# Performance work log

Hardware: AMD Instinct MI355X
Metric: run time of the kernel (lower is better)

The kernel has to match this reference:

```python
import jax, jax.numpy as jnp
import numpy as np

N = 100000      # num nodes
E = 1600000     # num edges (no self-loops; forward appends N self-loops)
DIN = 256       # in_channels
H = 1           # heads
C = 64          # out_channels per head
NEG = 0.2       # leaky_relu negative slope
NID = N // 10   # number of ID nodes


def setup_inputs() -> dict:
    key = jax.random.key(0)
    ks = jax.random.split(key, 7)
    x = jax.random.normal(ks[0], (N, DIN), jnp.float32)
    src = jax.random.randint(ks[1], (E,), 0, N, dtype=jnp.int32)
    off = jax.random.randint(ks[2], (E,), 1, N, dtype=jnp.int32)
    dst = ((src.astype(jnp.int64) + off.astype(jnp.int64)) % N).astype(jnp.int32)  # guarantees no self-loops
    edge_index = jnp.stack([src, dst])  # [2, E], row0 = source j, row1 = target i
    node_id = jax.random.randint(ks[3], (NID,), 0, N, dtype=jnp.int32)
    g = float(1.0 / np.sqrt(DIN))  # glorot-ish scale
    W = jax.random.uniform(ks[4], (DIN, H * C), jnp.float32, -g, g)
    W_id = jax.random.uniform(ks[5], (DIN, H * C), jnp.float32, -g, g)
    att = jax.random.uniform(ks[6], (1, H, 2 * C), jnp.float32, -g, g)
    return dict(x=x, edge_index=edge_index, node_id=node_id, W=W, W_id=W_id, att=att)


def _gat_id_forward(x, W, W_id, att, edge_index, node_id):
    # ID-aware transform: x @ W, plus extra W_id contribution added at id nodes
    x_id = x[node_id] @ W_id                      # [NID, H*C]
    h = x @ W                                     # [N, H*C]
    h = h.at[node_id].add(x_id)
    # add self-loops (inputs contain none)
    loops = jnp.arange(N, dtype=edge_index.dtype)
    src = jnp.concatenate([edge_index[0], loops])  # source j
    dst = jnp.concatenate([edge_index[1], loops])  # target i
    hr = h.reshape(N, H, C)
    xi = hr[dst]                                   # [Et, H, C]
    xj = hr[src]                                   # [Et, H, C]
    # alpha = (cat(x_i, x_j) * att).sum(-1)
    alpha = (xi * att[:, :, :C]).sum(-1) + (xj * att[:, :, C:]).sum(-1)  # [Et, H]
    alpha = jax.nn.leaky_relu(alpha, NEG)
    # segment softmax over target node (every node has a self-loop -> no empty segments)
    m = jax.ops.segment_max(alpha, dst, num_segments=N)
    alpha = jnp.exp(alpha - m[dst])
    s = jax.ops.segment_sum(alpha, dst, num_segments=N)
    alpha = alpha / (s[dst] + 1e-16)
    # dropout p=0 / eval mode -> no-op
    out = jax.ops.segment_sum(xj * alpha[:, :, None], dst, num_segments=N)  # [N, H, C]
    return out.reshape(N, H * C)  # concat=True, bias=False


def reference(x, edge_index, node_id, W, W_id, att):
    return _gat_id_forward(x, W, W_id, att, edge_index, node_id)
```

## Files before the change

kernel.cpp:

```cpp
#include <hip/hip_runtime.h>
#include <hip/hip_bf16.h>

#define N_NODES 100000
#define E_EDGES 1600000
#define DIN 256
#define C_OUT 64
#define NID_CNT 10000
#define NEG 0.2f
#define NBUCK 391
#define CAP 4608
#define GEMM_BLOCKS 391
#define BIN_BLOCKS 121
#define BIN_EPB 13224
#define BIN_ITERS 26

typedef short bf16x8 __attribute__((ext_vector_type(8)));
typedef float f32x4  __attribute__((ext_vector_type(4)));

__device__ __forceinline__ float lrelu(float x) { return x > 0.f ? x : NEG * x; }
__device__ __forceinline__ unsigned short f2bs(float f) {
    __hip_bfloat16 b = __float2bfloat16(f);
    return *reinterpret_cast<unsigned short*>(&b);
}
__device__ __forceinline__ bf16x8 pack8(float4 a, float4 b) {
    bf16x8 r;
    r[0] = (short)f2bs(a.x); r[1] = (short)f2bs(a.y);
    r[2] = (short)f2bs(a.z); r[3] = (short)f2bs(a.w);
    r[4] = (short)f2bs(b.x); r[5] = (short)f2bs(b.y);
    r[6] = (short)f2bs(b.z); r[7] = (short)f2bs(b.w);
    return r;
}
__device__ __forceinline__ float2 unpk2(unsigned u) {
    return make_float2(__uint_as_float(u << 16), __uint_as_float(u & 0xffff0000u));
}

__global__ __launch_bounds__(256) void k_zero(float* __restrict__ cnt,
                                              int* __restrict__ bkcur) {
    const int t = blockIdx.x * 256 + threadIdx.x;
    if (t < N_NODES) cnt[t] = 0.f;
    if (t < NBUCK) bkcur[t] = t * CAP;
}

__global__ __launch_bounds__(256) void k_prep(const float* __restrict__ W,
                                              const float* __restrict__ Wid,
                                              unsigned short* __restrict__ WtG,
                                              unsigned short* __restrict__ WidtG,
                                              const int* __restrict__ nid,
                                              float* __restrict__ cnt) {
    const int b = blockIdx.x;
    const int tid = threadIdx.x;
    if (b < 128) {
        const int t = b * 256 + tid;
        const int mat = t >> 14;
        const int r = t & 16383;
        const int k = r >> 6, c = r & 63;
        if (mat == 0) WtG[c * DIN + k] = f2bs(W[(long)k * C_OUT + c]);
        else          WidtG[c * DIN + k] = f2bs(Wid[(long)k * C_OUT + c]);
    } else {
        const int t = (b - 128) * 256 + tid;
        if (t < NID_CNT) atomicAdd(&cnt[nid[t]], 1.0f);
    }
}

__global__ __launch_bounds__(512, 4) void k_mega(const float* __restrict__ x,
                                                 const unsigned short* __restrict__ WtG,
                                                 const unsigned short* __restrict__ WidtG,
                                                 const float* __restrict__ cnt,
                                                 const float* __restrict__ att,
                                                 __hip_bfloat16* __restrict__ hb,
                                                 float* __restrict__ ad,
                                                 float* __restrict__ as,
                                                 const int* __restrict__ ei,
                                                 int* __restrict__ bkcur,
                                                 int2* __restrict__ binned) {
    __shared__ __align__(16) char smem[66560];
    const int blk = blockIdx.x;
    const int tid = threadIdx.x;

    if (blk < GEMM_BLOCKS) {
        char* wlds = smem;
        float* cnt_lds = (float*)(smem + 65536);
        const int w = tid >> 6, l = tid & 63;
        const int g = l >> 4, cl = l & 15;
        const int r0 = blk * 256;

        #pragma unroll
        for (int i = 0; i < 4; ++i) {
            int f = tid + i * 512;
            int c = f >> 5, s = f & 31;
            int byte = c * 512 + ((s ^ (c & 7)) << 4);
            *(bf16x8*)(wlds + byte)         = *(const bf16x8*)(WtG + (long)c * DIN + s * 8);
            *(bf16x8*)(wlds + 32768 + byte) = *(const bf16x8*)(WidtG + (long)c * DIN + s * 8);
        }
        if (tid < 256) cnt_lds[tid] = (r0 + tid < N_NODES) ? cnt[r0 + tid] : 0.f;
        __syncthreads();

        f32x4 acc1[2][4] = {};
        f32x4 acc2[2][4] = {};

        const int row0 = r0 + w * 32 + cl;
        const float* xp0 = x + (long)min(row0, N_NODES - 1) * DIN + g * 8;
        const float* xp1 = x + (long)min(row0 + 16, N_NODES - 1) * DIN + g * 8;

        float4 xb[2][4];
        xb[0][0] = *(const float4*)(xp0);
        xb[0][1] = *(const float4*)(xp0 + 4);
        xb[0][2] = *(const float4*)(xp1);
        xb[0][3] = *(const float4*)(xp1 + 4);
        #pragma unroll
        for (int kt = 0; kt < 8; ++kt) {
            if (kt < 7) {
                const int nb = (kt + 1) & 1;
                xb[nb][0] = *(const float4*)(xp0 + (kt + 1) * 32);
                xb[nb][1] = *(const float4*)(xp0 + (kt + 1) * 32 + 4);
                xb[nb][2] = *(const float4*)(xp1 + (kt + 1) * 32);
                xb[nb][3] = *(const float4*)(xp1 + (kt + 1) * 32 + 4);
            }
            const int cb = kt & 1;
            bf16x8 a0 = pack8(xb[cb][0], xb[cb][1]);
            bf16x8 a1 = pack8(xb[cb][2], xb[cb][3]);
            #pragma unroll
            for (int ct = 0; ct < 4; ++ct) {
                int c = ct * 16 + cl;
                int byte = c * 512 + (((kt * 4 + g) ^ (c & 7)) << 4);
                bf16x8 bw = *(const bf16x8*)(wlds + byte);
                bf16x8 bi = *(const bf16x8*)(wlds + 32768 + byte);
                acc1[0][ct] = __builtin_amdgcn_mfma_f32_16x16x32_bf16(a0, bw, acc1[0][ct], 0, 0, 0);
                acc1[1][ct] = __builtin_amdgcn_mfma_f32_16x16x32_bf16(a1, bw, acc1[1][ct], 0, 0, 0);
                acc2[0][ct] = __builtin_amdgcn_mfma_f32_16x16x32_bf16(a0, bi, acc2[0][ct], 0, 0, 0);
                acc2[1][ct] = __builtin_amdgcn_mfma_f32_16x16x32_bf16(a1, bi, acc2[1][ct], 0, 0, 0);
            }
        }
        __syncthreads();

        float attv1[4], attv2[4];
        #pragma unroll
        for (int ct = 0; ct < 4; ++ct) {
            attv1[ct] = att[ct * 16 + cl];
            attv2[ct] = att[C_OUT + ct * 16 + cl];
        }
        unsigned short* hbt = (unsigned short*)wlds;
        #pragma unroll
        for (int rt = 0; rt < 2; ++rt) {
            #pragma unroll
            for (int reg = 0; reg < 4; ++reg) {
                const int rbl = w * 32 + rt * 16 + g * 4 + reg;
                const float cv = cnt_lds[rbl];
                float pd = 0.f, ps = 0.f;
                #pragma unroll
                for (int ct = 0; ct < 4; ++ct) {
                    float hv = acc1[rt][ct][reg] + cv * acc2[rt][ct][reg];
                    pd += hv * attv1[ct];
                    ps += hv * attv2[ct];
                    hbt[rbl * 72 + ct * 16 + cl] = f2bs(hv);
                }
                #pragma unroll
                for (int o = 1; o < 16; o <<= 1) {
                    pd += __shfl_xor(pd, o, 64);
                    ps += __shfl_xor(ps, o, 64);
                }
                if (cl == 0) {
                    int grow = r0 + rbl;
                    if (grow < N_NODES) { ad[grow] = pd; as[grow] = ps; }
                }
            }
        }
        __syncthreads();
        #pragma unroll
        for (int i = 0; i < 4; ++i) {
            int f = tid + i * 512;
            int row = f >> 3, s = f & 7;
            int grow = r0 + row;
            if (grow < N_NODES) {
                bf16x8 v = *(const bf16x8*)(wlds + row * 144 + s * 16);
                *(bf16x8*)((unsigned short*)hb + (long)grow * C_OUT + s * 8) = v;
            }
        }
    } else {
        int* cnt_s = (int*)smem;
        int* base  = cnt_s + NBUCK;
        int* lcur  = base + NBUCK;
        const int b2 = blk - GEMM_BLOCKS;
        const int e0 = b2 * BIN_EPB;
        const int e1 = min(e0 + BIN_EPB, E_EDGES);
        for (int i = tid; i < NBUCK; i += 512) cnt_s[i] = 0;
        __syncthreads();
        int se[BIN_ITERS], de[BIN_ITERS];
        #pragma unroll
        for (int j = 0; j < BIN_ITERS; ++j) {
            int e = e0 + j * 512 + tid;
            if (e < e1) {
                se[j] = ei[e];
                de[j] = ei[E_EDGES + e];
                atomicAdd(&cnt_s[de[j] >> 8], 1);
            } else de[j] = -1;
        }
        __syncthreads();
        for (int i = tid; i < NBUCK; i += 512) {
            base[i] = cnt_s[i] ? atomicAdd(&bkcur[i], cnt_s[i]) : 0;
            lcur[i] = 0;
        }
        __syncthreads();
        #pragma unroll
        for (int j = 0; j < BIN_ITERS; ++j) {
            if (de[j] >= 0) {
                int bb = de[j] >> 8;
                int r = atomicAdd(&lcur[bb], 1);
                binned[base[bb] + r] = make_int2(se[j], de[j]);
            }
        }
    }
}

__global__ __launch_bounds__(256) void k_place(const int2* __restrict__ binned,
                                               const int* __restrict__ bkcur,
                                               int* __restrict__ csr,
                                               int* __restrict__ cur) {
    __shared__ int ncnt[256];
    __shared__ int tmp[256];
    __shared__ int ncur[256];
    const int tid = threadIdx.x;
    const int b = blockIdx.x;
    const int lo = b * CAP;
    const int n = bkcur[b] - lo;
    const int node0 = b << 8;
    ncnt[tid] = 0;
    __syncthreads();
    for (int e = tid; e < n; e += 256)
        atomicAdd(&ncnt[binned[lo + e].y - node0], 1);
    __syncthreads();
    const int v = ncnt[tid];
    tmp[tid] = v;
    __syncthreads();
    for (int o = 1; o < 256; o <<= 1) {
        int t = (tid >= o) ? tmp[tid - o] : 0;
        __syncthreads();
        tmp[tid] += t;
        __syncthreads();
    }
    const int incl = tmp[tid];
    if (node0 + tid < N_NODES) cur[node0 + tid] = lo + incl;
    ncur[tid] = incl - v;
    __syncthreads();
    for (int e = tid; e < n; e += 256) {
        int2 p = binned[lo + e];
        int r = atomicAdd(&ncur[p.y - node0], 1);
        csr[lo + r] = p.x;
    }
}

__global__ __launch_bounds__(256) void k_gather(const int* __restrict__ cur,
                                                const int* __restrict__ csr,
                                                const unsigned* __restrict__ hb2,
                                                const float* __restrict__ ad,
                                                const float* __restrict__ as,
                                                float* __restrict__ out) {
    const int lane = threadIdx.x & 63;
    const int lg = lane & 31;
    const int gb = lane & 32;
    const int i = blockIdx.x * 8 + ((threadIdx.x >> 6) << 1) + (lane >> 5);
    if (i >= N_NODES) return;
    const int end   = cur[i];
    const int start = (i & 255) ? cur[i - 1] : (i >> 8) * CAP;
    const int deg   = end - start;
    const float adi = ad[i];
    const float asi = as[i];
    float2 acc;
    float den;
    if (deg <= 32) {
        int s = 0; float a = -1e30f;
        if (lg < deg) { s = csr[start + lg]; a = as[s]; }
        float mx = fmaxf(a, asi);
        #pragma unroll
        for (int o = 16; o > 0; o >>= 1) mx = fmaxf(mx, __shfl_xor(mx, o, 64));
        const float m = lrelu(adi + mx);
        float w = (lg < deg) ? __expf(lrelu(adi + a) - m) : 0.f;
        const float wself = __expf(lrelu(adi + asi) - m);
        float wsum = w;
        #pragma unroll
        for (int o = 16; o > 0; o >>= 1) wsum += __shfl_xor(wsum, o, 64);
        den = wself + wsum;
        float2 hv = unpk2(hb2[(long)i * 32 + lg]);
        acc = make_float2(wself * hv.x, wself * hv.y);
        int j = 0;
        for (; j + 4 <= deg; j += 4) {
            int   s0 = __shfl(s, gb + j, 64),     s1 = __shfl(s, gb + j + 1, 64),
                  s2 = __shfl(s, gb + j + 2, 64), s3 = __shfl(s, gb + j + 3, 64);
            float w0 = __shfl(w, gb + j, 64),     w1 = __shfl(w, gb + j + 1, 64),
                  w2 = __shfl(w, gb + j + 2, 64), w3 = __shfl(w, gb + j + 3, 64);
            float2 h0 = unpk2(hb2[(long)s0 * 32 + lg]);
            float2 h1 = unpk2(hb2[(long)s1 * 32 + lg]);
            float2 h2 = unpk2(hb2[(long)s2 * 32 + lg]);
            float2 h3 = unpk2(hb2[(long)s3 * 32 + lg]);
            acc.x += w0 * h0.x; acc.y += w0 * h0.y;
            acc.x += w1 * h1.x; acc.y += w1 * h1.y;
            acc.x += w2 * h2.x; acc.y += w2 * h2.y;
            acc.x += w3 * h3.x; acc.y += w3 * h3.y;
        }
        for (; j < deg; ++j) {
            int   sj = __shfl(s, gb + j, 64);
            float wj = __shfl(w, gb + j, 64);
            float2 hj = unpk2(hb2[(long)sj * 32 + lg]);
            acc.x += wj * hj.x; acc.y += wj * hj.y;
        }
    } else {
        float mx = asi;
        for (int b = 0; b < deg; b += 32) {
            int idx = b + lg;
            if (idx < deg) mx = fmaxf(mx, as[csr[start + idx]]);
        }
        #pragma unroll
        for (int o = 16; o > 0; o >>= 1) mx = fmaxf(mx, __shfl_xor(mx, o, 64));
        const float m = lrelu(adi + mx);
        const float wself = __expf(lrelu(adi + asi) - m);
        float2 hv = unpk2(hb2[(long)i * 32 + lg]);
        acc = make_float2(wself * hv.x, wself * hv.y);
        den = wself;
        for (int b = 0; b < deg; b += 32) {
            int idx = b + lg;
            int s = 0; float w = 0.f;
            if (idx < deg) {
                s = csr[start + idx];
                w = __expf(lrelu(adi + as[s]) - m);
            }
            const int cnt2 = min(32, deg - b);
            for (int j = 0; j < cnt2; ++j) {
                int   sj = __shfl(s, gb + j, 64);
                float wj = __shfl(w, gb + j, 64);
                float2 hj = unpk2(hb2[(long)sj * 32 + lg]);
                acc.x += wj * hj.x; acc.y += wj * hj.y;
            }
            float wsum = w;
            #pragma unroll
            for (int o = 16; o > 0; o >>= 1) wsum += __shfl_xor(wsum, o, 64);
            den += wsum;
        }
    }
    const float r = 1.f / (den + 1e-16f);
    *(float2*)(out + (long)i * C_OUT + lg * 2) = make_float2(acc.x * r, acc.y * r);
}

extern "C" void kernel_launch(void* const* d_in, const int* in_sizes, int n_in,
                              void* d_out, int out_size, void* d_ws, size_t ws_size,
                              hipStream_t stream) {
    const float* x   = (const float*)d_in[0];
    const int*   ei  = (const int*)d_in[1];
    const int*   nid = (const int*)d_in[2];
    const float* W   = (const float*)d_in[3];
    const float* Wid = (const float*)d_in[4];
    const float* att = (const float*)d_in[5];
    float* out = (float*)d_out;

    char* ws = (char*)d_ws;
    __hip_bfloat16* hb = (__hip_bfloat16*)(ws);
    float* ad    = (float*)(ws + 12800000);
    float* as    = (float*)(ws + 13200000);
    float* cnt   = (float*)(ws + 13600000);
    int*   cur   = (int*)  (ws + 14000000);
    int2*  binned = (int2*)(ws + 14400000);
    int*   csr   = (int*)  (ws + 28900000);
    unsigned short* WtG  = (unsigned short*)(ws + 36200000);
    unsigned short* WidG = (unsigned short*)(ws + 36232768);
    int*   bkcur = (int*)  (ws + 36265536);

    k_zero<<<393, 256, 0, stream>>>(cnt, bkcur);
    k_prep<<<168, 256, 0, stream>>>(W, Wid, WtG, WidG, nid, cnt);
    k_mega<<<512, 512, 0, stream>>>(x, WtG, WidG, cnt, att, hb, ad, as, ei, bkcur, binned);
    k_place<<<NBUCK, 256, 0, stream>>>(binned, bkcur, csr, cur);
    k_gather<<<12500, 256, 0, stream>>>(cur, csr, (const unsigned*)hb, ad, as, out);
}
```

Baseline: 108.3 us.

## Compute W_id product only for ID nodes in a separate gather GEMM kernel

The main GEMM previously multiplied every row of x by both W and W_id and scaled the second product by a per-node count that is zero for most nodes. Now it computes only x@W over 128-row tiles with half the LDS and a higher occupancy bound. A new kernel gathers the ID-node rows, computes x@W + cnt·x@W_id for them, and overwrites hb, ad and as at those nodes. The binning path now re-reads edge indices from global memory instead of holding them in registers. The cost is an extra launch plus a scattered gather and overwrite, with duplicate ID nodes written redundantly.

```diff
diff --git a/kernel.cpp b/kernel.cpp
--- a/kernel.cpp
+++ b/kernel.cpp
@@ -9,10 +9,10 @@
 #define NEG 0.2f
 #define NBUCK 391
 #define CAP 4608
-#define GEMM_BLOCKS 391
-#define BIN_BLOCKS 121
-#define BIN_EPB 13224
-#define BIN_ITERS 26
+#define GEMM_BLOCKS 782
+#define BIN_BLOCKS 242
+#define BIN_EPB 6612
+#define ID_BLOCKS 79
 
 typedef short bf16x8 __attribute__((ext_vector_type(8)));
 typedef float f32x4  __attribute__((ext_vector_type(4)));
@@ -62,10 +62,8 @@
     }
 }
 
-__global__ __launch_bounds__(512, 4) void k_mega(const float* __restrict__ x,
+__global__ __launch_bounds__(512, 8) void k_mega(const float* __restrict__ x,
                                                  const unsigned short* __restrict__ WtG,
-                                                 const unsigned short* __restrict__ WidtG,
-                                                 const float* __restrict__ cnt,
                                                  const float* __restrict__ att,
                                                  __hip_bfloat16* __restrict__ hb,
                                                  float* __restrict__ ad,
@@ -73,62 +71,47 @@
                                                  const int* __restrict__ ei,
                                                  int* __restrict__ bkcur,
                                                  int2* __restrict__ binned) {
-    __shared__ __align__(16) char smem[66560];
+    __shared__ __align__(16) char smem[32768];
     const int blk = blockIdx.x;
     const int tid = threadIdx.x;
 
     if (blk < GEMM_BLOCKS) {
         char* wlds = smem;
-        float* cnt_lds = (float*)(smem + 65536);
         const int w = tid >> 6, l = tid & 63;
         const int g = l >> 4, cl = l & 15;
-        const int r0 = blk * 256;
+        const int r0 = blk * 128;
 
         #pragma unroll
         for (int i = 0; i < 4; ++i) {
             int f = tid + i * 512;
             int c = f >> 5, s = f & 31;
             int byte = c * 512 + ((s ^ (c & 7)) << 4);
-            *(bf16x8*)(wlds + byte)         = *(const bf16x8*)(WtG + (long)c * DIN + s * 8);
-            *(bf16x8*)(wlds + 32768 + byte) = *(const bf16x8*)(WidtG + (long)c * DIN + s * 8);
-        }
-        if (tid < 256) cnt_lds[tid] = (r0 + tid < N_NODES) ? cnt[r0 + tid] : 0.f;
-        __syncthreads();
-
-        f32x4 acc1[2][4] = {};
-        f32x4 acc2[2][4] = {};
-
-        const int row0 = r0 + w * 32 + cl;
+            *(bf16x8*)(wlds + byte) = *(const bf16x8*)(WtG + (long)c * DIN + s * 8);
+        }
+        __syncthreads();
+
+        f32x4 acc[4] = {};
+        const int row0 = r0 + w * 16 + cl;
         const float* xp0 = x + (long)min(row0, N_NODES - 1) * DIN + g * 8;
-        const float* xp1 = x + (long)min(row0 + 16, N_NODES - 1) * DIN + g * 8;
-
-        float4 xb[2][4];
+
+        float4 xb[2][2];
         xb[0][0] = *(const float4*)(xp0);
         xb[0][1] = *(const float4*)(xp0 + 4);
-        xb[0][2] = *(const float4*)(xp1);
-        xb[0][3] = *(const float4*)(xp1 + 4);
         #pragma unroll
         for (int kt = 0; kt < 8; ++kt) {
             if (kt < 7) {
                 const int nb = (kt + 1) & 1;
                 xb[nb][0] = *(const float4*)(xp0 + (kt + 1) * 32);
                 xb[nb][1] = *(const float4*)(xp0 + (kt + 1) * 32 + 4);
-                xb[nb][2] = *(const float4*)(xp1 + (kt + 1) * 32);
-                xb[nb][3] = *(const float4*)(xp1 + (kt + 1) * 32 + 4);
             }
             const int cb = kt & 1;
             bf16x8 a0 = pack8(xb[cb][0], xb[cb][1]);
-            bf16x8 a1 = pack8(xb[cb][2], xb[cb][3]);
             #pragma unroll
             for (int ct = 0; ct < 4; ++ct) {
                 int c = ct * 16 + cl;
                 int byte = c * 512 + (((kt * 4 + g) ^ (c & 7)) << 4);
                 bf16x8 bw = *(const bf16x8*)(wlds + byte);
-                bf16x8 bi = *(const bf16x8*)(wlds + 32768 + byte);
-                acc1[0][ct] = __builtin_amdgcn_mfma_f32_16x16x32_bf16(a0, bw, acc1[0][ct], 0, 0, 0);
-                acc1[1][ct] = __builtin_amdgcn_mfma_f32_16x16x32_bf16(a1, bw, acc1[1][ct], 0, 0, 0);
-                acc2[0][ct] = __builtin_amdgcn_mfma_f32_16x16x32_bf16(a0, bi, acc2[0][ct], 0, 0, 0);
-                acc2[1][ct] = __builtin_amdgcn_mfma_f32_16x16x32_bf16(a1, bi, acc2[1][ct], 0, 0, 0);
+                acc[ct] = __builtin_amdgcn_mfma_f32_16x16x32_bf16(a0, bw, acc[ct], 0, 0, 0);
             }
         }
         __syncthreads();
@@ -139,40 +122,36 @@
             attv1[ct] = att[ct * 16 + cl];
             attv2[ct] = att[C_OUT + ct * 16 + cl];
         }
-        unsigned short* hbt = (unsigned short*)wlds;
-        #pragma unroll
-        for (int rt = 0; rt < 2; ++rt) {
-            #pragma unroll
-            for (int reg = 0; reg < 4; ++reg) {
-                const int rbl = w * 32 + rt * 16 + g * 4 + reg;
-                const float cv = cnt_lds[rbl];
-                float pd = 0.f, ps = 0.f;
-                #pragma unroll
-                for (int ct = 0; ct < 4; ++ct) {
-                    float hv = acc1[rt][ct][reg] + cv * acc2[rt][ct][reg];
-                    pd += hv * attv1[ct];
-                    ps += hv * attv2[ct];
-                    hbt[rbl * 72 + ct * 16 + cl] = f2bs(hv);
-                }
-                #pragma unroll
-                for (int o = 1; o < 16; o <<= 1) {
-                    pd += __shfl_xor(pd, o, 64);
-                    ps += __shfl_xor(ps, o, 64);
-                }
-                if (cl == 0) {
-                    int grow = r0 + rbl;
-                    if (grow < N_NODES) { ad[grow] = pd; as[grow] = ps; }
-                }
-            }
-        }
-        __syncthreads();
-        #pragma unroll
-        for (int i = 0; i < 4; ++i) {
+        unsigned short* hbt = (unsigned short*)smem;
+        #pragma unroll
+        for (int reg = 0; reg < 4; ++reg) {
+            const int rbl = w * 16 + g * 4 + reg;
+            float pd = 0.f, ps = 0.f;
+            #pragma unroll
+            for (int ct = 0; ct < 4; ++ct) {
+                float hv = acc[ct][reg];
+                pd += hv * attv1[ct];
+                ps += hv * attv2[ct];
+                hbt[rbl * 72 + ct * 16 + cl] = f2bs(hv);
+            }
+            #pragma unroll
+            for (int o = 1; o < 16; o <<= 1) {
+                pd += __shfl_xor(pd, o, 64);
+                ps += __shfl_xor(ps, o, 64);
+            }
+            if (cl == 0) {
+                int grow = r0 + rbl;
+                if (grow < N_NODES) { ad[grow] = pd; as[grow] = ps; }
+            }
+        }
+        __syncthreads();
+        #pragma unroll
+        for (int i = 0; i < 2; ++i) {
             int f = tid + i * 512;
             int row = f >> 3, s = f & 7;
             int grow = r0 + row;
             if (grow < N_NODES) {
-                bf16x8 v = *(const bf16x8*)(wlds + row * 144 + s * 16);
+                bf16x8 v = *(const bf16x8*)(smem + row * 144 + s * 16);
                 *(bf16x8*)((unsigned short*)hb + (long)grow * C_OUT + s * 8) = v;
             }
         }
@@ -185,29 +164,128 @@
         const int e1 = min(e0 + BIN_EPB, E_EDGES);
         for (int i = tid; i < NBUCK; i += 512) cnt_s[i] = 0;
         __syncthreads();
-        int se[BIN_ITERS], de[BIN_ITERS];
-        #pragma unroll
-        for (int j = 0; j < BIN_ITERS; ++j) {
-            int e = e0 + j * 512 + tid;
-            if (e < e1) {
-                se[j] = ei[e];
-                de[j] = ei[E_EDGES + e];
-                atomicAdd(&cnt_s[de[j] >> 8], 1);
-            } else de[j] = -1;
-        }
+        for (int e = e0 + tid; e < e1; e += 512)
+            atomicAdd(&cnt_s[ei[E_EDGES + e] >> 8], 1);
         __syncthreads();
         for (int i = tid; i < NBUCK; i += 512) {
             base[i] = cnt_s[i] ? atomicAdd(&bkcur[i], cnt_s[i]) : 0;
             lcur[i] = 0;
         }
         __syncthreads();
-        #pragma unroll
-        for (int j = 0; j < BIN_ITERS; ++j) {
-            if (de[j] >= 0) {
-                int bb = de[j] >> 8;
-                int r = atomicAdd(&lcur[bb], 1);
-                binned[base[bb] + r] = make_int2(se[j], de[j]);
-            }
+        for (int e = e0 + tid; e < e1; e += 512) {
+            int s = ei[e];
+            int d = ei[E_EDGES + e];
+            int bb = d >> 8;
+            int r = atomicAdd(&lcur[bb], 1);
+            binned[base[bb] + r] = make_int2(s, d);
+        }
+    }
+}
+
+__global__ __launch_bounds__(256) void k_gemm_id(const float* __restrict__ x,
+                                                 const unsigned short* __restrict__ WtG,
+                                                 const unsigned short* __restrict__ WidtG,
+                                                 const float* __restrict__ cnt,
+                                                 const int* __restrict__ nid,
+                                                 const float* __restrict__ att,
+                                                 __hip_bfloat16* __restrict__ hb,
+                                                 float* __restrict__ ad,
+                                                 float* __restrict__ as) {
+    __shared__ __align__(16) char wlds[65536];
+    __shared__ int nodes[128];
+    __shared__ float cvs[128];
+    const int tid = threadIdx.x;
+    const int w = tid >> 6, l = tid & 63;
+    const int g = l >> 4, cl = l & 15;
+    const int r0 = blockIdx.x * 128;
+    if (tid < 128) {
+        int idx = r0 + tid;
+        int nd = (idx < NID_CNT) ? nid[idx] : -1;
+        nodes[tid] = nd;
+        cvs[tid] = (nd >= 0) ? cnt[nd] : 0.f;
+    }
+    #pragma unroll
+    for (int i = 0; i < 16; ++i) {
+        int f = tid + i * 256;
+        int half = f >> 11;
+        int ff = f & 2047;
+        int c = ff >> 5, s = ff & 31;
+        int byte = half * 32768 + c * 512 + ((s ^ (c & 7)) << 4);
+        const unsigned short* src = half ? WidtG : WtG;
+        *(bf16x8*)(wlds + byte) = *(const bf16x8*)(src + (long)c * DIN + s * 8);
+    }
+    __syncthreads();
+
+    const int n0 = nodes[w * 32 + cl];
+    const int n1 = nodes[w * 32 + 16 + cl];
+    const float* xp0 = x + (long)max(n0, 0) * DIN + g * 8;
+    const float* xp1 = x + (long)max(n1, 0) * DIN + g * 8;
+
+    f32x4 acc1[2][4] = {};
+    f32x4 acc2[2][4] = {};
+    #pragma unroll
+    for (int kt = 0; kt < 8; ++kt) {
+        float4 u0 = *(const float4*)(xp0 + kt * 32);
+        float4 u1 = *(const float4*)(xp0 + kt * 32 + 4);
+        float4 v0 = *(const float4*)(xp1 + kt * 32);
+        float4 v1 = *(const float4*)(xp1 + kt * 32 + 4);
+        bf16x8 a0 = pack8(u0, u1);
+        bf16x8 a1 = pack8(v0, v1);
+        #pragma unroll
+        for (int ct = 0; ct < 4; ++ct) {
+            int c = ct * 16 + cl;
+            int byte = c * 512 + (((kt * 4 + g) ^ (c & 7)) << 4);
+            bf16x8 bw = *(const bf16x8*)(wlds + byte);
+            bf16x8 bi = *(const bf16x8*)(wlds + 32768 + byte);
+            acc1[0][ct] = __builtin_amdgcn_mfma_f32_16x16x32_bf16(a0, bw, acc1[0][ct], 0, 0, 0);
+            acc1[1][ct] = __builtin_amdgcn_mfma_f32_16x16x32_bf16(a1, bw, acc1[1][ct], 0, 0, 0);
+            acc2[0][ct] = __builtin_amdgcn_mfma_f32_16x16x32_bf16(a0, bi, acc2[0][ct], 0, 0, 0);
+            acc2[1][ct] = __builtin_amdgcn_mfma_f32_16x16x32_bf16(a1, bi, acc2[1][ct], 0, 0, 0);
+        }
+    }
+    __syncthreads();
+
+    float attv1[4], attv2[4];
+    #pragma unroll
+    for (int ct = 0; ct < 4; ++ct) {
+        attv1[ct] = att[ct * 16 + cl];
+        attv2[ct] = att[C_OUT + ct * 16 + cl];
+    }
+    unsigned short* hbt = (unsigned short*)wlds;
+    #pragma unroll
+    for (int rt = 0; rt < 2; ++rt) {
+        #pragma unroll
+        for (int reg = 0; reg < 4; ++reg) {
+            const int rbl = w * 32 + rt * 16 + g * 4 + reg;
+            const float cv = cvs[rbl];
+            float pd = 0.f, ps = 0.f;
+            #pragma unroll
+            for (int ct = 0; ct < 4; ++ct) {
+                float hv = acc1[rt][ct][reg] + cv * acc2[rt][ct][reg];
+                pd += hv * attv1[ct];
+                ps += hv * attv2[ct];
+                hbt[rbl * 72 + ct * 16 + cl] = f2bs(hv);
+            }
+            #pragma unroll
+            for (int o = 1; o < 16; o <<= 1) {
+                pd += __shfl_xor(pd, o, 64);
+                ps += __shfl_xor(ps, o, 64);
+            }
+            if (cl == 0) {
+                int nd = nodes[rbl];
+                if (nd >= 0) { ad[nd] = pd; as[nd] = ps; }
+            }
+        }
+    }
+    __syncthreads();
+    #pragma unroll
+    for (int i = 0; i < 4; ++i) {
+        int f = tid + i * 256;
+        int row = f >> 3, s = f & 7;
+        int nd = nodes[row];
+        if (nd >= 0) {
+            bf16x8 v = *(const bf16x8*)(wlds + row * 144 + s * 16);
+            *(bf16x8*)((unsigned short*)hb + (long)nd * C_OUT + s * 8) = v;
         }
     }
 }
@@ -365,7 +443,9 @@
 
     k_zero<<<393, 256, 0, stream>>>(cnt, bkcur);
     k_prep<<<168, 256, 0, stream>>>(W, Wid, WtG, WidG, nid, cnt);
-    k_mega<<<512, 512, 0, stream>>>(x, WtG, WidG, cnt, att, hb, ad, as, ei, bkcur, binned);
+    k_mega<<<GEMM_BLOCKS + BIN_BLOCKS, 512, 0, stream>>>(x, WtG, att, hb, ad, as,
+                                                         ei, bkcur, binned);
+    k_gemm_id<<<ID_BLOCKS, 256, 0, stream>>>(x, WtG, WidG, cnt, nid, att, hb, ad, as);
     k_place<<<NBUCK, 256, 0, stream>>>(binned, bkcur, csr, cur);
     k_gather<<<12500, 256, 0, stream>>>(cur, csr, (const unsigned*)hb, ad, as, out);
 }
```

Result: slower. 119.0 us (+9.9%).
